# Kernel optimization log

Hardware: AMD Instinct MI355X
Metric: run time of the kernel (lower is better)

Reference implementation:

```python
import jax, jax.numpy as jnp
import numpy as np

SEQ, BATCH, HID = 4096, 32, 512


def setup_inputs() -> dict:
    key = jax.random.key(0)
    ks = jax.random.split(key, 7)
    s = 1.0 / np.sqrt(HID)
    return {
        "x0": jax.random.normal(ks[0], (SEQ, BATCH, 1), dtype=jnp.float32),
        "W_ih": jax.random.uniform(ks[1], (4 * HID, 1), jnp.float32, -s, s),
        "W_hh": jax.random.uniform(ks[2], (4 * HID, HID), jnp.float32, -s, s),
        "b_ih": jax.random.uniform(ks[3], (4 * HID,), jnp.float32, -s, s),
        "b_hh": jax.random.uniform(ks[4], (4 * HID,), jnp.float32, -s, s),
        "W_lin": jax.random.uniform(ks[5], (1, HID), jnp.float32, -s, s),
        "b_lin": jax.random.uniform(ks[6], (1,), jnp.float32, -s, s),
    }


def _lstm(x0, W_ih, W_hh, b_ih, b_hh):
    # x0: (T, B, 1). Precompute input contribution to gates for all steps.
    x_proj = jnp.einsum("tbi,gi->tbg", x0, W_ih) + (b_ih + b_hh)  # (T, B, 4H)
    T, B, _ = x_proj.shape
    H = W_hh.shape[1]
    h0 = jnp.zeros((B, H), x0.dtype)
    c0 = jnp.zeros((B, H), x0.dtype)

    def step(carry, xp):
        h, c = carry
        gates = xp + h @ W_hh.T  # (B, 4H)
        i, f, g, o = jnp.split(gates, 4, axis=-1)  # torch gate order i,f,g,o
        i = jax.nn.sigmoid(i)
        f = jax.nn.sigmoid(f)
        g = jnp.tanh(g)
        o = jax.nn.sigmoid(o)
        c = f * c + i * g
        h = o * jnp.tanh(c)
        return (h, c), h

    _, hs = jax.lax.scan(step, (h0, c0), x_proj)  # hs: (T, B, H)
    return hs


def reference(x0, W_ih, W_hh, b_ih, b_hh, W_lin, b_lin):
    hs = _lstm(x0, W_ih, W_hh, b_ih, b_hh)            # (T, B, H)
    y = jnp.einsum("tbh,oh->tbo", hs, W_lin) + b_lin  # (T, B, 1)
    return y + x0                                      # residual add
```

## Files before the change

kernel.cpp:

```cpp
#include <hip/hip_runtime.h>
#include <stdint.h>

#define T_STEPS 4096
#define BATCH 32
#define HID 512
#define GROUPS 8
#define BLK_THREADS 1024
#define NBLOCKS 256
#define SLOT_DW (BATCH * GROUPS * 64)

typedef _Float16 h2_t __attribute__((ext_vector_type(2)));
typedef uint32_t u32x8 __attribute__((ext_vector_type(8)));

__device__ inline uint32_t pack_h2(float a, float b) {
  h2_t v;
  v.x = (_Float16)a;
  v.y = (_Float16)b;
  return __builtin_bit_cast(uint32_t, v);
}

__device__ inline float fdot2(uint32_t a, uint32_t b, float c) {
  return __builtin_amdgcn_fdot2(__builtin_bit_cast(h2_t, a),
                                __builtin_bit_cast(h2_t, b), c, false);
}

__device__ inline uint32_t aread(uint32_t a) {
  uint32_t v;
  asm("v_accvgpr_read_b32 %0, %1" : "=v"(v) : "a"(a));
  return v;
}

__device__ inline uint64_t uni64(const void* p) {
  uint32_t lo = __builtin_amdgcn_readfirstlane((uint32_t)(uintptr_t)p);
  uint32_t hi = __builtin_amdgcn_readfirstlane((uint32_t)((uintptr_t)p >> 32));
  return ((uint64_t)hi << 32) | lo;
}

__device__ inline void kinv() {
  asm volatile("s_dcache_inv" ::: "memory");
}

__device__ inline void sload_rec(uint64_t p, u32x8* d0, u32x8* d1,
                                 u32x8* d2, u32x8* d3,
                                 uint32_t* t0, uint32_t* t1,
                                 uint32_t* t2, uint32_t* t3) {
  asm volatile("s_load_dwordx8 %0, %8, 0x0\n\t"
               "s_load_dword %4, %8, 0x20\n\t"
               "s_load_dwordx8 %1, %8, 0x40\n\t"
               "s_load_dword %5, %8, 0x60\n\t"
               "s_load_dwordx8 %2, %8, 0x80\n\t"
               "s_load_dword %6, %8, 0xa0\n\t"
               "s_load_dwordx8 %3, %8, 0xc0\n\t"
               "s_load_dword %7, %8, 0xe0\n\t"
               "s_waitcnt lgkmcnt(0)"
               : "=&s"(*d0), "=&s"(*d1), "=&s"(*d2), "=&s"(*d3),
                 "=&s"(*t0), "=&s"(*t1), "=&s"(*t2), "=&s"(*t3)
               : "s"(p) : "memory");
}

__device__ inline float sigf(float x) { return 1.0f / (1.0f + __expf(-x)); }
__device__ inline float tanh_fast(float x) {
  float a = fabsf(x);
  float e = __expf(-2.0f * a);
  float r = (1.0f - e) / (1.0f + e);
  return copysignf(r, x);
}

__global__ __launch_bounds__(BLK_THREADS)
void lstm_tagline(const float* __restrict__ x0,
                  const float* __restrict__ W_ih,
                  const float* __restrict__ W_hh,
                  const float* __restrict__ b_ih,
                  const float* __restrict__ b_hh,
                  const float* __restrict__ W_lin,
                  const float* __restrict__ b_lin,
                  float* __restrict__ y,
                  uint32_t* __restrict__ h_ex,
                  int* __restrict__ claim)
{
  __shared__ float x0_lds[T_STEPS];
  __shared__ float ylds[T_STEPS];
  __shared__ float gacc[2][256];
  __shared__ int s_bg;

  const int tid = threadIdx.x;

  if (tid == 0) {
    uint32_t xcc;
    asm volatile("s_getreg_b32 %0, hwreg(HW_REG_XCC_ID)" : "=s"(xcc));
    xcc &= 7;
    int slot = atomicAdd(claim + xcc * 16, 1);
    s_bg = (slot < 32) ? (int)(((4 * xcc + (slot >> 3)) << 3) | (slot & 7))
                       : -1;
  }
  __syncthreads();
  if (s_bg < 0) return;
  const int b  = s_bg >> 3;
  const int g  = s_bg & 7;
  const int u0 = g * 64;
  const int wv = tid >> 6;
  const int rg = wv >> 3;
  const int cs = wv & 7;
  const int l  = tid & 63;

  uint32_t a0[32], a1[32];
  {
    const int r0 = 128 * rg + l;
    const int r1 = r0 + 64;
    const int R0 = (r0 >> 6) * HID + u0 + (r0 & 63);
    const int R1 = (r1 >> 6) * HID + u0 + (r1 & 63);
    const float2* p0 = (const float2*)(W_hh + (size_t)R0 * HID + 64 * cs);
    const float2* p1 = (const float2*)(W_hh + (size_t)R1 * HID + 64 * cs);
#pragma unroll
    for (int k = 0; k < 32; ++k) {
      float2 a = p0[k], c = p1[k];
      uint32_t t0 = pack_h2(a.x, a.y);
      uint32_t t1 = pack_h2(c.x, c.y);
      asm("v_accvgpr_write_b32 %0, %1" : "=a"(a0[k]) : "v"(t0));
      asm("v_accvgpr_write_b32 %0, %1" : "=a"(a1[k]) : "v"(t1));
    }
  }
  for (int i = tid; i < T_STEPS; i += BLK_THREADS) {
    x0_lds[i] = x0[i * BATCH + b];
    ylds[i] = 0.f;
  }
  if (tid < 256) { gacc[0][tid] = 0.f; gacc[1][tid] = 0.f; }

  float c_state = 0.f;
  float wih_[4] = {0.f, 0.f, 0.f, 0.f}, bs_[4] = {0.f, 0.f, 0.f, 0.f};
  float wlin_u = 0.f, blin = 0.f;
  if (tid < 64) {
#pragma unroll
    for (int j = 0; j < 4; ++j) {
      int R = j * HID + u0 + tid;
      wih_[j] = W_ih[R];
      bs_[j] = b_ih[R] + b_hh[R];
    }
    wlin_u = W_lin[u0 + tid];
    blin = b_lin[0];
  }

  uint32_t* hb = h_ex + (size_t)b * (GROUPS * 64);
  const uint64_t dpu[2] = { uni64(hb + 64 * cs),
                            uni64(hb + SLOT_DW + 64 * cs) };
  uint32_t* pub01[2] = { hb + 64 * g, hb + SLOT_DW + 64 * g };

  __syncthreads();

  int dead = 0;
  for (int t = 0; t < T_STEPS; ++t) {
    const int sl = t & 1, ns = sl ^ 1;

    u32x8 D0, D1, D2, D3;
    uint32_t tg0, tg1, tg2, tg3;
    {
      const uint32_t want = (uint32_t)t;
      int guard = 0;
      for (;;) {
        kinv();
        sload_rec(dpu[sl], &D0, &D1, &D2, &D3, &tg0, &tg1, &tg2, &tg3);
        if ((tg0 == want) & (tg1 == want) &
            (tg2 == want) & (tg3 == want)) break;
        if (dead || ++guard > (1 << 18)) { dead = 1; break; }
        __builtin_amdgcn_s_sleep(1);
      }
    }

    float acc0a = 0.f, acc0b = 0.f, acc1a = 0.f, acc1b = 0.f;
#pragma unroll
    for (int k = 0; k < 8; ++k) {
      acc0a = fdot2(aread(a0[k]),      D0[k], acc0a);
      acc1a = fdot2(aread(a1[k]),      D0[k], acc1a);
      acc0b = fdot2(aread(a0[8 + k]),  D1[k], acc0b);
      acc1b = fdot2(aread(a1[8 + k]),  D1[k], acc1b);
      acc0a = fdot2(aread(a0[16 + k]), D2[k], acc0a);
      acc1a = fdot2(aread(a1[16 + k]), D2[k], acc1a);
      acc0b = fdot2(aread(a0[24 + k]), D3[k], acc0b);
      acc1b = fdot2(aread(a1[24 + k]), D3[k], acc1b);
    }
    atomicAdd(&gacc[sl][128 * rg + l], acc0a + acc0b);
    atomicAdd(&gacc[sl][128 * rg + 64 + l], acc1a + acc1b);
    __syncthreads();

    if (tid < 64) {
      const float xv = x0_lds[t];
      float gi = gacc[sl][tid]       + xv * wih_[0] + bs_[0];
      float gf = gacc[sl][tid + 64]  + xv * wih_[1] + bs_[1];
      float gg = gacc[sl][tid + 128] + xv * wih_[2] + bs_[2];
      float go = gacc[sl][tid + 192] + xv * wih_[3] + bs_[3];
      float si = sigf(gi), sf = sigf(gf), tg_ = tanh_fast(gg), so = sigf(go);
      c_state = sf * c_state + si * tg_;
      float h = so * tanh_fast(c_state);

      float hn = __shfl_down(h, 1, 64);
      uint32_t val = 0;
      int doff = 0;
      bool act = false;
      if ((tid & 1) == 0) {
        int j = tid >> 1;
        val = pack_h2(h, hn);
        doff = ((j >> 3) << 4) + (j & 7);
        act = true;
      } else if (tid < 8) {
        int L = (tid - 1) >> 1;
        val = (uint32_t)(t + 1);
        doff = (L << 4) + 8;
        act = true;
      }
      if (act) pub01[ns][doff] = val;

      gacc[sl][tid] = 0.f;
      gacc[sl][tid + 64] = 0.f;
      gacc[sl][tid + 128] = 0.f;
      gacc[sl][tid + 192] = 0.f;

      float p = wlin_u * h;
#pragma unroll
      for (int m = 32; m >= 1; m >>= 1) p += __shfl_xor(p, m, 64);
      if (tid == 0) ylds[t] = p;
    }
  }

  __syncthreads();
  for (int i = tid; i < T_STEPS; i += BLK_THREADS) {
    float val = ylds[i];
    if (g == 0) val += blin + x0_lds[i];
    unsafeAtomicAdd(&y[i * BATCH + b], val);
  }
}

extern "C" void kernel_launch(void* const* d_in, const int* in_sizes, int n_in,
                              void* d_out, int out_size, void* d_ws, size_t ws_size,
                              hipStream_t stream) {
  const float* x0    = (const float*)d_in[0];
  const float* W_ih  = (const float*)d_in[1];
  const float* W_hh  = (const float*)d_in[2];
  const float* b_ih  = (const float*)d_in[3];
  const float* b_hh  = (const float*)d_in[4];
  const float* W_lin = (const float*)d_in[5];
  const float* b_lin = (const float*)d_in[6];
  float* y = (float*)d_out;

  uint32_t* h_ex = (uint32_t*)d_ws;
  int* claim     = (int*)(h_ex + 2 * SLOT_DW);
  const size_t init_bytes = (size_t)2 * SLOT_DW * sizeof(uint32_t)
                            + 8 * 16 * sizeof(int);

  (void)hipMemsetAsync(d_ws, 0, init_bytes, stream);
  (void)hipMemsetAsync(d_out, 0, (size_t)out_size * sizeof(float), stream);

  hipLaunchKernelGGL(lstm_tagline, dim3(NBLOCKS), dim3(BLK_THREADS), 0, stream,
                     x0, W_ih, W_hh, b_ih, b_hh, W_lin, b_lin, y, h_ex, claim);
}
```

Before: 14.49 ms.

## Replace per-step block barrier with LDS arrival counter and priority hints

Drops the per-step __syncthreads and uses an LDS arrival counter that only wave 0 spins on before the gate nonlinearities. The other 15 waves can go straight to polling for the next step's hidden state. It also keeps the fp16 weights in ordinary VGPRs instead of AGPRs, which removes the accvgpr reads, and adds s_setprio around the critical sections while changing the sleep and guard values. The counter ordering leaves room for a race: wave 0 resets arrive[sl] and clears gacc without a barrier, and that slot is reused two steps later. Holding the weights in VGPRs also raises register pressure at 1024 threads.

```diff
diff --git a/kernel.cpp b/kernel.cpp
--- a/kernel.cpp
+++ b/kernel.cpp
@@ -22,12 +22,6 @@
 __device__ inline float fdot2(uint32_t a, uint32_t b, float c) {
   return __builtin_amdgcn_fdot2(__builtin_bit_cast(h2_t, a),
                                 __builtin_bit_cast(h2_t, b), c, false);
-}
-
-__device__ inline uint32_t aread(uint32_t a) {
-  uint32_t v;
-  asm("v_accvgpr_read_b32 %0, %1" : "=v"(v) : "a"(a));
-  return v;
 }
 
 __device__ inline uint64_t uni64(const void* p) {
@@ -67,20 +61,21 @@
 }
 
 __global__ __launch_bounds__(BLK_THREADS)
-void lstm_tagline(const float* __restrict__ x0,
-                  const float* __restrict__ W_ih,
-                  const float* __restrict__ W_hh,
-                  const float* __restrict__ b_ih,
-                  const float* __restrict__ b_hh,
-                  const float* __restrict__ W_lin,
-                  const float* __restrict__ b_lin,
-                  float* __restrict__ y,
-                  uint32_t* __restrict__ h_ex,
-                  int* __restrict__ claim)
+void lstm_nobar(const float* __restrict__ x0,
+                const float* __restrict__ W_ih,
+                const float* __restrict__ W_hh,
+                const float* __restrict__ b_ih,
+                const float* __restrict__ b_hh,
+                const float* __restrict__ W_lin,
+                const float* __restrict__ b_lin,
+                float* __restrict__ y,
+                uint32_t* __restrict__ h_ex,
+                int* __restrict__ claim)
 {
   __shared__ float x0_lds[T_STEPS];
   __shared__ float ylds[T_STEPS];
   __shared__ float gacc[2][256];
+  __shared__ int arrive[2];
   __shared__ int s_bg;
 
   const int tid = threadIdx.x;
@@ -103,7 +98,7 @@
   const int cs = wv & 7;
   const int l  = tid & 63;
 
-  uint32_t a0[32], a1[32];
+  uint32_t w0[32], w1[32];
   {
     const int r0 = 128 * rg + l;
     const int r1 = r0 + 64;
@@ -114,10 +109,8 @@
 #pragma unroll
     for (int k = 0; k < 32; ++k) {
       float2 a = p0[k], c = p1[k];
-      uint32_t t0 = pack_h2(a.x, a.y);
-      uint32_t t1 = pack_h2(c.x, c.y);
-      asm("v_accvgpr_write_b32 %0, %1" : "=a"(a0[k]) : "v"(t0));
-      asm("v_accvgpr_write_b32 %0, %1" : "=a"(a1[k]) : "v"(t1));
+      w0[k] = pack_h2(a.x, a.y);
+      w1[k] = pack_h2(c.x, c.y);
     }
   }
   for (int i = tid; i < T_STEPS; i += BLK_THREADS) {
@@ -125,6 +118,7 @@
     ylds[i] = 0.f;
   }
   if (tid < 256) { gacc[0][tid] = 0.f; gacc[1][tid] = 0.f; }
+  if (tid < 2) arrive[tid] = 0;
 
   float c_state = 0.f;
   float wih_[4] = {0.f, 0.f, 0.f, 0.f}, bs_[4] = {0.f, 0.f, 0.f, 0.f};
@@ -161,28 +155,41 @@
         sload_rec(dpu[sl], &D0, &D1, &D2, &D3, &tg0, &tg1, &tg2, &tg3);
         if ((tg0 == want) & (tg1 == want) &
             (tg2 == want) & (tg3 == want)) break;
-        if (dead || ++guard > (1 << 18)) { dead = 1; break; }
-        __builtin_amdgcn_s_sleep(1);
+        if (dead || ++guard > (1 << 17)) { dead = 1; break; }
+        __builtin_amdgcn_s_sleep(2);
       }
     }
 
+    __builtin_amdgcn_s_setprio(1);
     float acc0a = 0.f, acc0b = 0.f, acc1a = 0.f, acc1b = 0.f;
 #pragma unroll
     for (int k = 0; k < 8; ++k) {
-      acc0a = fdot2(aread(a0[k]),      D0[k], acc0a);
-      acc1a = fdot2(aread(a1[k]),      D0[k], acc1a);
-      acc0b = fdot2(aread(a0[8 + k]),  D1[k], acc0b);
-      acc1b = fdot2(aread(a1[8 + k]),  D1[k], acc1b);
-      acc0a = fdot2(aread(a0[16 + k]), D2[k], acc0a);
-      acc1a = fdot2(aread(a1[16 + k]), D2[k], acc1a);
-      acc0b = fdot2(aread(a0[24 + k]), D3[k], acc0b);
-      acc1b = fdot2(aread(a1[24 + k]), D3[k], acc1b);
+      acc0a = fdot2(w0[k],      D0[k], acc0a);
+      acc1a = fdot2(w1[k],      D0[k], acc1a);
+      acc0b = fdot2(w0[8 + k],  D1[k], acc0b);
+      acc1b = fdot2(w1[8 + k],  D1[k], acc1b);
+      acc0a = fdot2(w0[16 + k], D2[k], acc0a);
+      acc1a = fdot2(w1[16 + k], D2[k], acc1a);
+      acc0b = fdot2(w0[24 + k], D3[k], acc0b);
+      acc1b = fdot2(w1[24 + k], D3[k], acc1b);
     }
     atomicAdd(&gacc[sl][128 * rg + l], acc0a + acc0b);
     atomicAdd(&gacc[sl][128 * rg + 64 + l], acc1a + acc1b);
-    __syncthreads();
+    asm volatile("" ::: "memory");
+    if (l == 0) atomicAdd(&arrive[sl], 1);
+    __builtin_amdgcn_s_setprio(0);
 
     if (tid < 64) {
+      {
+        int guard = 0;
+        while (((volatile int*)arrive)[sl] < 16) {
+          if (++guard > (1 << 20)) break;
+        }
+      }
+      asm volatile("" ::: "memory");
+      __builtin_amdgcn_s_setprio(1);
+      arrive[sl] = 0;
+
       const float xv = x0_lds[t];
       float gi = gacc[sl][tid]       + xv * wih_[0] + bs_[0];
       float gf = gacc[sl][tid + 64]  + xv * wih_[1] + bs_[1];
@@ -218,6 +225,7 @@
 #pragma unroll
       for (int m = 32; m >= 1; m >>= 1) p += __shfl_xor(p, m, 64);
       if (tid == 0) ylds[t] = p;
+      __builtin_amdgcn_s_setprio(0);
     }
   }
 
@@ -249,6 +257,6 @@
   (void)hipMemsetAsync(d_ws, 0, init_bytes, stream);
   (void)hipMemsetAsync(d_out, 0, (size_t)out_size * sizeof(float), stream);
 
-  hipLaunchKernelGGL(lstm_tagline, dim3(NBLOCKS), dim3(BLK_THREADS), 0, stream,
+  hipLaunchKernelGGL(lstm_nobar, dim3(NBLOCKS), dim3(BLK_THREADS), 0, stream,
                      x0, W_ih, W_hh, b_ih, b_hh, W_lin, b_lin, y, h_ex, claim);
 }
```

Result: faster. 13.98 ms (-3.5%).
